# Kernel tuning notes

Hardware: AMD Instinct MI355X
Metric: run time of the kernel (lower is better)

The kernel has to match this reference:

```python
import jax, jax.numpy as jnp
import numpy as np


def setup_inputs() -> dict:
    key = jax.random.key(0)
    k1, k2 = jax.random.split(key)
    x = jax.random.normal(k1, (16384, 1024), dtype=jnp.float32)
    # 10 butterfly stages, each with 512 independent 2x2 mixing matrices
    Ws = jax.random.normal(k2, (10, 512, 2, 2), dtype=jnp.float32)
    return {"x": x, "Ws": Ws}


def reference(x, Ws):
    """PairLinear_MixerBlock forward for input_dim == output_dim == 2^L.
    selector and reducer are Identity; only the butterfly mixing stages remain.
    """
    bs, dim = x.shape
    n_stages = Ws.shape[0]  # log2(dim)
    y = x
    for i in range(n_stages):
        stride = 2 ** i
        # y.view(-1, 2, 2**i).permute(0, 2, 1).contiguous().view(bs, -1)
        y = y.reshape(-1, 2, stride).transpose(0, 2, 1).reshape(bs, -1)
        # PairLinear: view(bs, -1, 2) then per-pair 2x2 matmul with Ws[i]
        y = jnp.einsum('bpk,pkj->bpj', y.reshape(bs, -1, 2), Ws[i]).reshape(bs, -1)
        # y.view(-1, 2**i, 2).permute(0, 2, 1).contiguous()
        y = y.reshape(-1, stride, 2).transpose(0, 2, 1).reshape(bs, dim)
    return y
```

## Files before the change

### kernel.cpp

```cpp
#include <hip/hip_runtime.h>

#define DIM 1024
#define RPW 2
#define WAVES 4
#define ROWS_PER_BLOCK (RPW * WAVES)
#define NSTEP 24
#define PACKED_BYTES (NSTEP * 64 * 8 * 4)
#define WLDS_FLOATS (NSTEP * 64 * 8)

typedef float f32x4 __attribute__((ext_vector_type(4)));


__global__ void pack_weights(const float* __restrict__ Ws, float* __restrict__ pw) {
    int t = blockIdx.x * blockDim.x + threadIdx.x;
    if (t >= NSTEP * 64) return;
    int lane = t & 63;
    int step = t >> 6;
    int q = step & 3;
    int i = (step >> 2) + 2;
    int m = 1 << (i - 2);
    int a = (lane >> (i - 2)) & 1;
    int P0 = (((q * 64 + lane) >> (i - 1)) << i) | ((lane & (m - 1)) << 2);
    const float4* Wm = (const float4*)Ws;
    float4 wa, wb;
    float* pa = (float*)&wa;
    float* pb = (float*)&wb;
    #pragma unroll
    for (int e = 0; e < 4; ++e) {
        float4 M = Wm[i * 512 + P0 + e];
        pa[e] = a ? M.w : M.x;
        pb[e] = a ? M.y : M.z;
    }
    ((float4*)pw)[t] = wa;
    ((float4*)pw)[(WLDS_FLOATS / 8) + t] = wb;
}

template <bool PACKED>
__global__ __launch_bounds__(256) void butterfly_kernel(
    const float* __restrict__ x,
    const float* __restrict__ Ws,
    const float* __restrict__ pw,
    float* __restrict__ out,
    int rows)
{
    const int lane = threadIdx.x & 63;
    const int wave = threadIdx.x >> 6;
    const int row0 = (blockIdx.x * WAVES + wave) * RPW;

    const float4* __restrict__ Wm = (const float4*)Ws;

    __shared__ float wlds[WLDS_FLOATS];

    float d[RPW][16];

    #pragma unroll
    for (int r = 0; r < RPW; ++r) {
        int row = row0 + r;
        if (row < rows) {
            const f32x4* src = (const f32x4*)(x + (size_t)row * DIM);
            #pragma unroll
            for (int q = 0; q < 4; ++q) {
                f32x4 v = __builtin_nontemporal_load(&src[q * 64 + lane]);
                d[r][q*4+0] = v.x; d[r][q*4+1] = v.y;
                d[r][q*4+2] = v.z; d[r][q*4+3] = v.w;
            }
        } else {
            #pragma unroll
            for (int e = 0; e < 16; ++e) d[r][e] = 0.f;
        }
    }

    if (PACKED) {
        #pragma unroll
        for (int k = 0; k < 12; ++k) {
            int chunk = wave * 12 + k;
            const float* g = pw + chunk * 256 + lane * 4;
            float* l = &wlds[chunk * 256 + lane * 4];
            __builtin_amdgcn_global_load_lds(g, l, 16, 0, 0);
        }
        __syncthreads();
    }

    #pragma unroll
    for (int q = 0; q < 4; ++q) {
        int base = 0*512 + q*128 + lane*2;
        float4 m0 = Wm[base], m1 = Wm[base+1];
        #pragma unroll
        for (int r = 0; r < RPW; ++r) {
            int e = q*4;
            float u = d[r][e+0], v = d[r][e+1];
            d[r][e+0] = u*m0.x + v*m0.z;
            d[r][e+1] = u*m0.y + v*m0.w;
            u = d[r][e+2]; v = d[r][e+3];
            d[r][e+2] = u*m1.x + v*m1.z;
            d[r][e+3] = u*m1.y + v*m1.w;
        }
    }

    #pragma unroll
    for (int q = 0; q < 4; ++q) {
        int base = 1*512 + q*128 + lane*2;
        float4 m0 = Wm[base], m1 = Wm[base+1];
        #pragma unroll
        for (int r = 0; r < RPW; ++r) {
            int e = q*4;
            float u = d[r][e+0], v = d[r][e+2];
            d[r][e+0] = u*m0.x + v*m0.z;
            d[r][e+2] = u*m0.y + v*m0.w;
            u = d[r][e+1]; v = d[r][e+3];
            d[r][e+1] = u*m1.x + v*m1.z;
            d[r][e+3] = u*m1.y + v*m1.w;
        }
    }

    #pragma unroll
    for (int i = 2; i < 8; ++i) {
        const int m = 1 << (i - 2);
        #pragma unroll
        for (int q = 0; q < 4; ++q) {
            const int step = (i - 2) * 4 + q;
            float wA0, wA1, wA2, wA3, wB0, wB1, wB2, wB3;
            if (PACKED) {
                f32x4 wa = *(const f32x4*)&wlds[(step * 64 + lane) * 4];
                f32x4 wb = *(const f32x4*)&wlds[(WLDS_FLOATS / 2) + (step * 64 + lane) * 4];
                wA0 = wa.x; wA1 = wa.y; wA2 = wa.z; wA3 = wa.w;
                wB0 = wb.x; wB1 = wb.y; wB2 = wb.z; wB3 = wb.w;
            } else {
                const int a = (lane >> (i - 2)) & 1;
                int P0 = (((q*64 + lane) >> (i-1)) << i) | ((lane & (m-1)) << 2);
                int base = i*512 + P0;
                float4 M0 = Wm[base+0], M1 = Wm[base+1], M2 = Wm[base+2], M3 = Wm[base+3];
                wA0 = a ? M0.w : M0.x; wB0 = a ? M0.y : M0.z;
                wA1 = a ? M1.w : M1.x; wB1 = a ? M1.y : M1.z;
                wA2 = a ? M2.w : M2.x; wB2 = a ? M2.y : M2.z;
                wA3 = a ? M3.w : M3.x; wB3 = a ? M3.y : M3.z;
            }
            #pragma unroll
            for (int r = 0; r < RPW; ++r) {
                int e = q*4;
                float o0 = __shfl_xor(d[r][e+0], m);
                float o1 = __shfl_xor(d[r][e+1], m);
                float o2 = __shfl_xor(d[r][e+2], m);
                float o3 = __shfl_xor(d[r][e+3], m);
                d[r][e+0] = d[r][e+0]*wA0 + o0*wB0;
                d[r][e+1] = d[r][e+1]*wA1 + o1*wB1;
                d[r][e+2] = d[r][e+2]*wA2 + o2*wB2;
                d[r][e+3] = d[r][e+3]*wA3 + o3*wB3;
            }
        }
    }

    #pragma unroll
    for (int qp = 0; qp < 2; ++qp) {
        int base = 8*512 + qp*256 + lane*4;
        float4 M0 = Wm[base+0], M1 = Wm[base+1], M2 = Wm[base+2], M3 = Wm[base+3];
        #pragma unroll
        for (int r = 0; r < RPW; ++r) {
            int eu = (2*qp)*4, ev = (2*qp+1)*4;
            float u, v;
            u = d[r][eu+0]; v = d[r][ev+0]; d[r][eu+0] = u*M0.x + v*M0.z; d[r][ev+0] = u*M0.y + v*M0.w;
            u = d[r][eu+1]; v = d[r][ev+1]; d[r][eu+1] = u*M1.x + v*M1.z; d[r][ev+1] = u*M1.y + v*M1.w;
            u = d[r][eu+2]; v = d[r][ev+2]; d[r][eu+2] = u*M2.x + v*M2.z; d[r][ev+2] = u*M2.y + v*M2.w;
            u = d[r][eu+3]; v = d[r][ev+3]; d[r][eu+3] = u*M3.x + v*M3.z; d[r][ev+3] = u*M3.y + v*M3.w;
        }
    }

    #pragma unroll
    for (int qp = 0; qp < 2; ++qp) {
        int base = 9*512 + qp*256 + lane*4;
        float4 M0 = Wm[base+0], M1 = Wm[base+1], M2 = Wm[base+2], M3 = Wm[base+3];
        #pragma unroll
        for (int r = 0; r < RPW; ++r) {
            int eu = qp*4, ev = (qp+2)*4;
            float u, v;
            u = d[r][eu+0]; v = d[r][ev+0]; d[r][eu+0] = u*M0.x + v*M0.z; d[r][ev+0] = u*M0.y + v*M0.w;
            u = d[r][eu+1]; v = d[r][ev+1]; d[r][eu+1] = u*M1.x + v*M1.z; d[r][ev+1] = u*M1.y + v*M1.w;
            u = d[r][eu+2]; v = d[r][ev+2]; d[r][eu+2] = u*M2.x + v*M2.z; d[r][ev+2] = u*M2.y + v*M2.w;
            u = d[r][eu+3]; v = d[r][ev+3]; d[r][eu+3] = u*M3.x + v*M3.z; d[r][ev+3] = u*M3.y + v*M3.w;
        }
    }

    #pragma unroll
    for (int r = 0; r < RPW; ++r) {
        int row = row0 + r;
        if (row < rows) {
            f32x4* dst = (f32x4*)(out + (size_t)row * DIM);
            #pragma unroll
            for (int q = 0; q < 4; ++q) {
                f32x4 v;
                v.x = d[r][q*4+0]; v.y = d[r][q*4+1];
                v.z = d[r][q*4+2]; v.w = d[r][q*4+3];
                __builtin_nontemporal_store(v, &dst[q * 64 + lane]);
            }
        }
    }
}

extern "C" void kernel_launch(void* const* d_in, const int* in_sizes, int n_in,
                              void* d_out, int out_size, void* d_ws, size_t ws_size,
                              hipStream_t stream) {
    const float* x  = (const float*)d_in[0];
    const float* Ws = (const float*)d_in[1];
    float* out = (float*)d_out;

    int rows = in_sizes[0] / DIM;
    int grid = (rows + ROWS_PER_BLOCK - 1) / ROWS_PER_BLOCK;

    if (ws_size >= (size_t)PACKED_BYTES) {
        float* pw = (float*)d_ws;
        pack_weights<<<6, 256, 0, stream>>>(Ws, pw);
        butterfly_kernel<true><<<grid, 256, 0, stream>>>(x, Ws, pw, out, rows);
    } else {
        butterfly_kernel<false><<<grid, 256, 0, stream>>>(x, Ws, nullptr, out, rows);
    }
}
```

Before: 43.50 us.

## Process four row-pairs per wave with double-buffered register prefetch

Each wave now handles four row-pairs instead of one, ping-ponging between two register buffers so the next pair's global loads are issued before the current pair is computed and stored. This amortizes the per-block weight LDS load and sync over more rows and overlaps load latency with compute. The nontemporal hint on loads is dropped. The cost is higher register pressure from two live 32-float buffers, a quarter as many blocks, and loss of handling for an odd row count.

```diff
diff --git a/kernel.cpp b/kernel.cpp
--- a/kernel.cpp
+++ b/kernel.cpp
@@ -3,7 +3,7 @@
 #define DIM 1024
 #define RPW 2
 #define WAVES 4
-#define ROWS_PER_BLOCK (RPW * WAVES)
+#define TPW 4
 #define NSTEP 24
 #define PACKED_BYTES (NSTEP * 64 * 8 * 4)
 #define WLDS_FLOATS (NSTEP * 64 * 8)
@@ -35,52 +35,40 @@
     ((float4*)pw)[(WLDS_FLOATS / 8) + t] = wb;
 }
 
+__device__ __forceinline__ void load_pair(const float* __restrict__ x, int pair,
+                                          int lane, float (&d)[RPW][16]) {
+    const f32x4* src = (const f32x4*)(x + (size_t)pair * RPW * DIM);
+    #pragma unroll
+    for (int r = 0; r < RPW; ++r) {
+        #pragma unroll
+        for (int q = 0; q < 4; ++q) {
+            f32x4 v = src[r * 256 + q * 64 + lane];
+            d[r][q*4+0] = v.x; d[r][q*4+1] = v.y;
+            d[r][q*4+2] = v.z; d[r][q*4+3] = v.w;
+        }
+    }
+}
+
+__device__ __forceinline__ void store_pair(float* __restrict__ out, int pair,
+                                           int lane, float (&d)[RPW][16]) {
+    f32x4* dst = (f32x4*)(out + (size_t)pair * RPW * DIM);
+    #pragma unroll
+    for (int r = 0; r < RPW; ++r) {
+        #pragma unroll
+        for (int q = 0; q < 4; ++q) {
+            f32x4 v;
+            v.x = d[r][q*4+0]; v.y = d[r][q*4+1];
+            v.z = d[r][q*4+2]; v.w = d[r][q*4+3];
+            __builtin_nontemporal_store(v, &dst[r * 256 + q * 64 + lane]);
+        }
+    }
+}
+
 template <bool PACKED>
-__global__ __launch_bounds__(256) void butterfly_kernel(
-    const float* __restrict__ x,
-    const float* __restrict__ Ws,
-    const float* __restrict__ pw,
-    float* __restrict__ out,
-    int rows)
-{
-    const int lane = threadIdx.x & 63;
-    const int wave = threadIdx.x >> 6;
-    const int row0 = (blockIdx.x * WAVES + wave) * RPW;
-
-    const float4* __restrict__ Wm = (const float4*)Ws;
-
-    __shared__ float wlds[WLDS_FLOATS];
-
-    float d[RPW][16];
-
-    #pragma unroll
-    for (int r = 0; r < RPW; ++r) {
-        int row = row0 + r;
-        if (row < rows) {
-            const f32x4* src = (const f32x4*)(x + (size_t)row * DIM);
-            #pragma unroll
-            for (int q = 0; q < 4; ++q) {
-                f32x4 v = __builtin_nontemporal_load(&src[q * 64 + lane]);
-                d[r][q*4+0] = v.x; d[r][q*4+1] = v.y;
-                d[r][q*4+2] = v.z; d[r][q*4+3] = v.w;
-            }
-        } else {
-            #pragma unroll
-            for (int e = 0; e < 16; ++e) d[r][e] = 0.f;
-        }
-    }
-
-    if (PACKED) {
-        #pragma unroll
-        for (int k = 0; k < 12; ++k) {
-            int chunk = wave * 12 + k;
-            const float* g = pw + chunk * 256 + lane * 4;
-            float* l = &wlds[chunk * 256 + lane * 4];
-            __builtin_amdgcn_global_load_lds(g, l, 16, 0, 0);
-        }
-        __syncthreads();
-    }
-
+__device__ __forceinline__ void compute_pair(float (&d)[RPW][16],
+                                             const float4* __restrict__ Wm,
+                                             const float* __restrict__ wsrc,
+                                             int lane) {
     #pragma unroll
     for (int q = 0; q < 4; ++q) {
         int base = 0*512 + q*128 + lane*2;
@@ -121,8 +109,8 @@
             const int step = (i - 2) * 4 + q;
             float wA0, wA1, wA2, wA3, wB0, wB1, wB2, wB3;
             if (PACKED) {
-                f32x4 wa = *(const f32x4*)&wlds[(step * 64 + lane) * 4];
-                f32x4 wb = *(const f32x4*)&wlds[(WLDS_FLOATS / 2) + (step * 64 + lane) * 4];
+                f32x4 wa = *(const f32x4*)&wsrc[(step * 64 + lane) * 4];
+                f32x4 wb = *(const f32x4*)&wsrc[(WLDS_FLOATS / 2) + (step * 64 + lane) * 4];
                 wA0 = wa.x; wA1 = wa.y; wA2 = wa.z; wA3 = wa.w;
                 wB0 = wb.x; wB1 = wb.y; wB2 = wb.z; wB3 = wb.w;
             } else {
@@ -179,21 +167,55 @@
             u = d[r][eu+3]; v = d[r][ev+3]; d[r][eu+3] = u*M3.x + v*M3.z; d[r][ev+3] = u*M3.y + v*M3.w;
         }
     }
-
-    #pragma unroll
-    for (int r = 0; r < RPW; ++r) {
-        int row = row0 + r;
-        if (row < rows) {
-            f32x4* dst = (f32x4*)(out + (size_t)row * DIM);
-            #pragma unroll
-            for (int q = 0; q < 4; ++q) {
-                f32x4 v;
-                v.x = d[r][q*4+0]; v.y = d[r][q*4+1];
-                v.z = d[r][q*4+2]; v.w = d[r][q*4+3];
-                __builtin_nontemporal_store(v, &dst[q * 64 + lane]);
-            }
-        }
-    }
+}
+
+template <bool PACKED>
+__global__ __launch_bounds__(256) void butterfly_kernel(
+    const float* __restrict__ x,
+    const float* __restrict__ Ws,
+    const float* __restrict__ pw,
+    float* __restrict__ out,
+    int npairs)
+{
+    const int lane = threadIdx.x & 63;
+    const int wave = threadIdx.x >> 6;
+    const int g = blockIdx.x * WAVES + wave;
+    const int p0 = g * TPW;
+
+    const float4* __restrict__ Wm = (const float4*)Ws;
+
+    __shared__ float wlds[WLDS_FLOATS];
+
+    if (PACKED) {
+        #pragma unroll
+        for (int k = 0; k < 12; ++k) {
+            int chunk = wave * 12 + k;
+            const float* gsrc = pw + chunk * 256 + lane * 4;
+            float* l = &wlds[chunk * 256 + lane * 4];
+            __builtin_amdgcn_global_load_lds(gsrc, l, 16, 0, 0);
+        }
+    }
+
+    float dA[RPW][16], dB[RPW][16];
+
+    const bool h0 = (p0 + 0) < npairs;
+    const bool h1 = (p0 + 1) < npairs;
+    const bool h2 = (p0 + 2) < npairs;
+    const bool h3 = (p0 + 3) < npairs;
+
+    if (h0) load_pair(x, p0 + 0, lane, dA);
+    if (PACKED) __syncthreads();
+
+    if (h1) load_pair(x, p0 + 1, lane, dB);
+    if (h0) { compute_pair<PACKED>(dA, Wm, wlds, lane); store_pair(out, p0 + 0, lane, dA); }
+
+    if (h2) load_pair(x, p0 + 2, lane, dA);
+    if (h1) { compute_pair<PACKED>(dB, Wm, wlds, lane); store_pair(out, p0 + 1, lane, dB); }
+
+    if (h3) load_pair(x, p0 + 3, lane, dB);
+    if (h2) { compute_pair<PACKED>(dA, Wm, wlds, lane); store_pair(out, p0 + 2, lane, dA); }
+
+    if (h3) { compute_pair<PACKED>(dB, Wm, wlds, lane); store_pair(out, p0 + 3, lane, dB); }
 }
 
 extern "C" void kernel_launch(void* const* d_in, const int* in_sizes, int n_in,
@@ -204,13 +226,15 @@
     float* out = (float*)d_out;
 
     int rows = in_sizes[0] / DIM;
-    int grid = (rows + ROWS_PER_BLOCK - 1) / ROWS_PER_BLOCK;
+    int npairs = rows / RPW;
+    int pairs_per_block = WAVES * TPW;
+    int grid = (npairs + pairs_per_block - 1) / pairs_per_block;
 
     if (ws_size >= (size_t)PACKED_BYTES) {
         float* pw = (float*)d_ws;
         pack_weights<<<6, 256, 0, stream>>>(Ws, pw);
-        butterfly_kernel<true><<<grid, 256, 0, stream>>>(x, Ws, pw, out, rows);
+        butterfly_kernel<true><<<grid, 256, 0, stream>>>(x, Ws, pw, out, npairs);
     } else {
-        butterfly_kernel<false><<<grid, 256, 0, stream>>>(x, Ws, nullptr, out, rows);
-    }
-}
+        butterfly_kernel<false><<<grid, 256, 0, stream>>>(x, Ws, nullptr, out, npairs);
+    }
+}
```

New measurement: 52.79 us. +21.3%, slower.
